# Performance work log

Measured on AMD Instinct MI355X. Metric: run time of the kernel, lower is better.

The kernel has to match this reference:

```python
import jax, jax.numpy as jnp
import numpy as np

B, T, F = 32, 128, 128      # batch, time, num_features
NF = 8                      # num_filters
KW = 5                      # kernel_width
NC = F * NF                 # num_cells = 1024
NCLS = 1000                 # num_classes
PAD = KW // 2
EPS = 1e-5


def setup_inputs() -> dict:
    key = jax.random.key(0)
    ks = jax.random.split(key, 12)
    rn = lambda k, shape, s=1.0: jax.random.normal(k, shape, dtype=jnp.float32) * s
    st = (B, NF, 1, NC)
    zc = lambda: jnp.zeros((NF,), jnp.float32)
    oc = lambda: jnp.ones((NF,), jnp.float32)
    inp = {
        "x": rn(ks[0], (B, T, F)),
        "s": rn(ks[1], st),                       # init=1.0 -> std 1 normal
        "n": jnp.zeros(st, jnp.float32),
        "d": jnp.zeros(st, jnp.float32),
        "h": jnp.zeros(st, jnp.float32),
        "a_max": jnp.full(st, -1e38, jnp.float32),  # torch fills a_max with -1e38
        "x_resize_w": rn(ks[2], (NC, F), 0.05),     # Linear(num_features->num_cells), no bias
        "g_w": rn(ks[3], (NF, NF + 1, 1, KW), 0.1), "g_b": zc(), "g_gamma": oc(), "g_beta": zc(),
        "u_w": rn(ks[4], (NF, 1, 1, KW), 0.1),      "u_b": zc(), "u_gamma": oc(), "u_beta": zc(),
        "a_w": rn(ks[5], (NF, NF + 1, 1, KW), 0.1), "a_b": zc(), "a_gamma": oc(), "a_beta": zc(),
        "dec_w": rn(ks[6], (NF, NF + 1, 1, KW), 0.1), "dec_b": zc(), "dec_gamma": oc(), "dec_beta": zc(),
        "o_w": rn(ks[7], (NCLS, NC * NF), 0.01),
        "o_b": jnp.zeros((NCLS,), jnp.float32),
    }
    return inp


def _conv(x, w, b):
    # x: [B, C_in, 1, NC]; w: [C_out, C_in, 1, KW]; 'same' padding on width (kw odd)
    y = jax.lax.conv_general_dilated(x, w, window_strides=(1, 1),
                                     padding=[(0, 0), (PAD, PAD)],
                                     dimension_numbers=("NCHW", "OIHW", "NCHW"))
    return y + b[None, :, None, None]


def _bn(x, gamma, beta):
    # BatchNorm2d in training mode: per-channel batch stats over (N, H, W), biased var
    mu = jnp.mean(x, axis=(0, 2, 3), keepdims=True)
    var = jnp.mean((x - mu) ** 2, axis=(0, 2, 3), keepdims=True)
    return gamma[None, :, None, None] * (x - mu) * jax.lax.rsqrt(var + EPS) + beta[None, :, None, None]


def reference(x, s, n, d, h, a_max,
              x_resize_w,
              g_w, g_b, g_gamma, g_beta,
              u_w, u_b, u_gamma, u_beta,
              a_w, a_b, a_gamma, a_beta,
              dec_w, dec_b, dec_gamma, dec_beta,
              o_w, o_b):
    h0 = h + jnp.tanh(s)

    def step(carry, x_t):
        h_t, n_t, d_t, am = carry
        xr = (x_t @ x_resize_w.T)[:, None, None, :]    # [B,1,1,NC]
        xh = jnp.concatenate([xr, h_t], axis=1)        # [B,NF+1,1,NC]
        g_t = _bn(_conv(xh, g_w, g_b), g_gamma, g_beta)
        u_t = _bn(_conv(xr, u_w, u_b), u_gamma, u_beta)
        a_t = _bn(_conv(xh, a_w, a_b), a_gamma, a_beta)
        dec = jax.nn.sigmoid(_bn(_conv(xh, dec_w, dec_b), dec_gamma, dec_beta))
        ed = jnp.exp(-dec)
        z_t = u_t * jnp.tanh(g_t)
        a_new = jnp.maximum(am * ed, a_t)              # torch: max(a_max*exp(-decay), a_t)
        exp_diff = jnp.exp(am - a_new)
        exp_scaled = jnp.exp(a_t - a_new)
        n_new = n_t * ed * exp_diff + z_t * exp_scaled
        d_new = d_t * ed * exp_diff + exp_scaled
        h_new = jnp.tanh(n_new / d_new)
        return (h_new, n_new, d_new, a_new), None

    (h_T, n_T, d_T, am_T), _ = jax.lax.scan(step, (h0, n, d, a_max), jnp.swapaxes(x, 0, 1))
    outs = h_T.reshape(h_T.shape[0], -1) @ o_w.T + o_b  # [B, NCLS]
    return (outs, s, n_T, d_T, h_T, am_T)
```

## Files before the change

kernel.cpp:

```cpp
#include <hip/hip_runtime.h>


#define NBLK 256
#define NTHR 512

constexpr int Bb = 32, Tt = 128, NCc = 1024;
constexpr int PROW = 1032;
constexpr float EPSf  = 1e-5f;
constexpr float INV_N = 1.0f / 32768.0f;

constexpr size_t XR_OFF  = 0;
constexpr size_t XR_SZ   = (size_t)Tt * Bb * PROW;
constexpr size_t WT_OFF  = XR_OFF + XR_SZ;
constexpr size_t WT_SZ   = 131072;
constexpr size_t WPK_OFF = WT_OFF + WT_SZ;
constexpr size_t WPK_SZ  = 1280;
constexpr size_t ACC_OFF = WPK_OFF + WPK_SZ;
constexpr size_t ACC_SZ  = 3 * 4 * 64 * 32;
constexpr size_t SL2_OFF = ACC_OFF + ACC_SZ;
constexpr size_t SL2_SZ  = 2 * 32 * 8 * 2 * 64;
constexpr size_t CNT_OFF = SL2_OFF + SL2_SZ;

constexpr int OUT_S  = 32000;
constexpr int OUT_N  = 294144;
constexpr int OUT_D  = 556288;
constexpr int OUT_H  = 818432;
constexpr int OUT_AM = 1080576;

__device__ __forceinline__ float fast_tanh(float x) {
  float e = __expf(2.0f * x);
  return 1.0f - 2.0f / (e + 1.0f);
}

__global__ void prep_kernel(const float* __restrict__ w, float* __restrict__ wT,
                            const float* __restrict__ gw, const float* __restrict__ aw,
                            const float* __restrict__ dw, const float* __restrict__ uw,
                            float* __restrict__ wpack, float* __restrict__ acc3,
                            unsigned* __restrict__ cnt) {
  const int g = blockIdx.x * 256 + threadIdx.x;
  if (g < 131072) {
    const int c = g >> 7, k = g & 127;
    wT[k * 1024 + c] = w[g];
  }
  if (g < 1280) {
    const int f = g / 160, r = g % 160, ci = r >> 4, k = r & 15;
    float v = 0.f;
    if (ci < 9) {
      if (k < 5)       v = gw[(f * 9 + ci) * 5 + k];
      else if (k < 10) v = aw[(f * 9 + ci) * 5 + (k - 5)];
      else if (k < 15) v = dw[(f * 9 + ci) * 5 + (k - 10)];
    } else {
      if (k < 5)       v = uw[f * 5 + k];
    }
    wpack[g] = v;
  }
  if (g < (int)ACC_SZ) acc3[g] = 0.f;
  if (g < 1024) cnt[g] = 0u;
}

__global__ void __launch_bounds__(256) xr_kernel(const float* __restrict__ x,
                                                 const float* __restrict__ wT,
                                                 float* __restrict__ XR) {
  const int tb0 = blockIdx.x * 16;
  const int c0  = threadIdx.x * 4;
  float4 acc[16];
#pragma unroll
  for (int j = 0; j < 16; ++j) acc[j] = make_float4(0.f, 0.f, 0.f, 0.f);
#pragma unroll 4
  for (int k = 0; k < 128; ++k) {
    const float4 wv = *(const float4*)(wT + (size_t)k * 1024 + c0);
#pragma unroll
    for (int j = 0; j < 16; ++j) {
      const int tb = tb0 + j;
      const float xs = x[(size_t)(tb & 31) * 16384 + (size_t)(tb >> 5) * 128 + k];
      acc[j].x = fmaf(xs, wv.x, acc[j].x);
      acc[j].y = fmaf(xs, wv.y, acc[j].y);
      acc[j].z = fmaf(xs, wv.z, acc[j].z);
      acc[j].w = fmaf(xs, wv.w, acc[j].w);
    }
  }
#pragma unroll
  for (int j = 0; j < 16; ++j) {
    float* row = XR + (size_t)(tb0 + j) * PROW;
    *(float4*)(row + 4 + c0) = acc[j];
    if (threadIdx.x == 0)   { row[0] = row[1] = row[2] = row[3] = 0.f; }
    if (threadIdx.x == 255) { row[1028] = row[1029] = row[1030] = row[1031] = 0.f; }
  }
}

__global__ void __launch_bounds__(NTHR) scan_kernel(
    const float* __restrict__ XR, const float* __restrict__ wpack,
    float* acc3, float* slots2, unsigned* cnt,
    const float* __restrict__ s_in, const float* __restrict__ n_in,
    const float* __restrict__ d_in, const float* __restrict__ h_in,
    const float* __restrict__ am_in,
    const float* __restrict__ ggm, const float* __restrict__ gbt,
    const float* __restrict__ ugm, const float* __restrict__ ubt,
    const float* __restrict__ agm, const float* __restrict__ abt,
    const float* __restrict__ dgm, const float* __restrict__ dbt,
    float* __restrict__ out)
{
  const int bb   = (int)blockIdx.x >> 3;
  const int cc   = (int)blockIdx.x & 7;
  const int tid  = (int)threadIdx.x;
  const int w    = tid >> 6;
  const int lane = tid & 63;
  const int fu   = __builtin_amdgcn_readfirstlane(w);
  const float* __restrict__ wpk = wpack + fu * 160;

  const int c0   = 2 * lane;
  const int gc0  = cc * 128 + c0;
  const int cellbase = bb * 8192 + w * 1024 + gc0;
  const int rep  = (int)blockIdx.x & 3;

  const float ggamma = ggm[fu], gbeta = gbt[fu];
  const float ugamma = ugm[fu], ubeta = ubt[fu];
  const float agamma = agm[fu], abeta = abt[fu];
  const float dgamma = dgm[fu], dbeta = dbt[fu];

  __shared__ float hl[8][136];

  float nst[2], dst[2], amst[2], hv[2];
  float hn = 0.f, hd = 0.f, ham = -1e38f;
  const int  hloc   = (lane < 2) ? (lane - 2) : (128 + (lane - 2));
  const bool hvalid = (lane < 4) && ((lane < 2) ? (cc > 0) : (cc < 7));
  {
    const float2 n2 = *(const float2*)(n_in  + cellbase);
    const float2 d2 = *(const float2*)(d_in  + cellbase);
    const float2 a2 = *(const float2*)(am_in + cellbase);
    const float2 h2 = *(const float2*)(h_in  + cellbase);
    const float2 s2 = *(const float2*)(s_in  + cellbase);
    nst[0] = n2.x; nst[1] = n2.y;
    dst[0] = d2.x; dst[1] = d2.y;
    amst[0] = a2.x; amst[1] = a2.y;
    hv[0] = h2.x + fast_tanh(s2.x);
    hv[1] = h2.y + fast_tanh(s2.y);
    *(float2*)&hl[w][c0 + 4] = make_float2(hv[0], hv[1]);

    float hh0 = 0.f;
    if (hvalid) {
      const int gcell = bb * 8192 + w * 1024 + cc * 128 + hloc;
      hn  = n_in[gcell]; hd = d_in[gcell]; ham = am_in[gcell];
      hh0 = h_in[gcell] + fast_tanh(s_in[gcell]);
    }
    if (lane < 4) hl[w][hloc + 4] = hh0;
    if (lane >= 4 && lane < 8) {
      const int pidx = (lane == 4) ? 0 : (lane == 5) ? 1 : (lane == 6) ? 134 : 135;
      hl[w][pidx] = 0.f;
    }
  }
  __syncthreads();

  for (int t = 0; t < Tt; ++t) {
    const int p2 = t & 1;
    const int p3 = t % 3;

    float accg[2] = {0.f, 0.f}, acca[2] = {0.f, 0.f};
    float accd[2] = {0.f, 0.f}, accu[2] = {0.f, 0.f};

    const float2* xr2 = (const float2*)(XR + (size_t)(t * Bb + bb) * PROW + 2 + gc0);
    const float2 xa = xr2[0], xb = xr2[1], xc = xr2[2];

#pragma unroll
    for (int r = 0; r < 8; ++r) {
      const float2 qa = *(const float2*)&hl[r][c0 + 2];
      const float2 qb = *(const float2*)&hl[r][c0 + 4];
      const float2 qc = *(const float2*)&hl[r][c0 + 6];
      const float w6[6] = {qa.x, qa.y, qb.x, qb.y, qc.x, qc.y};
      const float* wp = wpk + (r + 1) * 16;
#pragma unroll
      for (int kw = 0; kw < 5; ++kw) {
        const float wg = wp[kw], wa = wp[5 + kw], wd = wp[10 + kw];
#pragma unroll
        for (int j = 0; j < 2; ++j) {
          const float v = w6[j + kw];
          accg[j] = fmaf(v, wg, accg[j]);
          acca[j] = fmaf(v, wa, acca[j]);
          accd[j] = fmaf(v, wd, accd[j]);
        }
      }
    }
    {
      const float w6[6] = {xa.x, xa.y, xb.x, xb.y, xc.x, xc.y};
      const float* wp = wpk;
      const float* wu = wpk + 144;
#pragma unroll
      for (int kw = 0; kw < 5; ++kw) {
        const float wg = wp[kw], wa = wp[5 + kw], wd = wp[10 + kw], wv = wu[kw];
#pragma unroll
        for (int j = 0; j < 2; ++j) {
          const float v = w6[j + kw];
          accg[j] = fmaf(v, wg, accg[j]);
          acca[j] = fmaf(v, wa, acca[j]);
          accd[j] = fmaf(v, wd, accd[j]);
          accu[j] = fmaf(v, wv, accu[j]);
        }
      }
    }

    {
      float ps[8];
      ps[0] = accg[0] + accg[1]; ps[1] = fmaf(accg[0], accg[0], accg[1] * accg[1]);
      ps[2] = acca[0] + acca[1]; ps[3] = fmaf(acca[0], acca[0], acca[1] * acca[1]);
      ps[4] = accd[0] + accd[1]; ps[5] = fmaf(accd[0], accd[0], accd[1] * accd[1]);
      ps[6] = accu[0] + accu[1]; ps[7] = fmaf(accu[0], accu[0], accu[1] * accu[1]);
#pragma unroll
      for (int k = 0; k < 8; ++k) {
        float v = ps[k];
#pragma unroll
        for (int m = 1; m <= 32; m <<= 1) v += __shfl_xor(v, m);
        ps[k] = v;
      }
      float myv = ps[0];
#pragma unroll
      for (int k = 1; k < 8; ++k) if (lane == k) myv = ps[k];
      if (lane < 8)
        __hip_atomic_fetch_add(acc3 + p3 * 8192 + rep * 2048 + (w * 8 + lane) * 32,
                               myv, __ATOMIC_RELAXED, __HIP_MEMORY_SCOPE_AGENT);
    }

    if (lane == 0 || lane == 63) {
      const int side = lane ? 1 : 0;
      float* bs = slots2 + ((((size_t)p2 * 32 + bb) * 8 + cc) * 2 + side) * 64 + w * 8;
      __hip_atomic_store(bs + 0, accg[0], __ATOMIC_RELAXED, __HIP_MEMORY_SCOPE_AGENT);
      __hip_atomic_store(bs + 1, accg[1], __ATOMIC_RELAXED, __HIP_MEMORY_SCOPE_AGENT);
      __hip_atomic_store(bs + 2, acca[0], __ATOMIC_RELAXED, __HIP_MEMORY_SCOPE_AGENT);
      __hip_atomic_store(bs + 3, acca[1], __ATOMIC_RELAXED, __HIP_MEMORY_SCOPE_AGENT);
      __hip_atomic_store(bs + 4, accd[0], __ATOMIC_RELAXED, __HIP_MEMORY_SCOPE_AGENT);
      __hip_atomic_store(bs + 5, accd[1], __ATOMIC_RELAXED, __HIP_MEMORY_SCOPE_AGENT);
      __hip_atomic_store(bs + 6, accu[0], __ATOMIC_RELAXED, __HIP_MEMORY_SCOPE_AGENT);
      __hip_atomic_store(bs + 7, accu[1], __ATOMIC_RELAXED, __HIP_MEMORY_SCOPE_AGENT);
    }

    asm volatile("s_waitcnt vmcnt(0)" ::: "memory");
    __syncthreads();
    if (tid == 0) {
      unsigned* leaf = cnt + ((blockIdx.x >> 4) * 32);
      unsigned* root = cnt + 16 * 32;
      unsigned* gen  = cnt + 17 * 32;
      const unsigned tgt = (unsigned)(t + 1);
      const unsigned old =
          __hip_atomic_fetch_add(leaf, 1u, __ATOMIC_RELAXED, __HIP_MEMORY_SCOPE_AGENT);
      if (old == 16u * tgt - 1u) {
        const unsigned old2 =
            __hip_atomic_fetch_add(root, 1u, __ATOMIC_RELAXED, __HIP_MEMORY_SCOPE_AGENT);
        if (old2 == 16u * tgt - 1u)
          __hip_atomic_store(gen, tgt, __ATOMIC_RELAXED, __HIP_MEMORY_SCOPE_AGENT);
      }
      while (__hip_atomic_load(gen, __ATOMIC_RELAXED, __HIP_MEMORY_SCOPE_AGENT) < tgt)
        __builtin_amdgcn_s_sleep(1);
    }
    __syncthreads();

    float st[8];
    {
      float sv = 0.f;
      if (lane < 8) {
        const float* ap = acc3 + p3 * 8192 + (w * 8 + lane) * 32;
#pragma unroll
        for (int r = 0; r < 4; ++r)
          sv += __hip_atomic_load(ap + r * 2048, __ATOMIC_RELAXED, __HIP_MEMORY_SCOPE_AGENT);
      }
#pragma unroll
      for (int k = 0; k < 8; ++k) st[k] = __shfl(sv, k);
    }
    if (blockIdx.x == 0 && tid < 256)
      __hip_atomic_store(acc3 + ((t + 2) % 3) * 8192 + tid * 32, 0.f,
                         __ATOMIC_RELAXED, __HIP_MEMORY_SCOPE_AGENT);

    const float mg = st[0] * INV_N; const float vg = fmaf(-mg, mg, st[1] * INV_N);
    const float sg = ggamma * rsqrtf(vg + EPSf); const float og = fmaf(-mg, sg, gbeta);
    const float ma = st[2] * INV_N; const float va = fmaf(-ma, ma, st[3] * INV_N);
    const float sa = agamma * rsqrtf(va + EPSf); const float oa = fmaf(-ma, sa, abeta);
    const float md = st[4] * INV_N; const float vd = fmaf(-md, md, st[5] * INV_N);
    const float sd = dgamma * rsqrtf(vd + EPSf); const float od = fmaf(-md, sd, dbeta);
    const float mu = st[6] * INV_N; const float vu = fmaf(-mu, mu, st[7] * INV_N);
    const float su = ugamma * rsqrtf(vu + EPSf); const float ou = fmaf(-mu, su, ubeta);

#pragma unroll
    for (int j = 0; j < 2; ++j) {
      const float gb = fmaf(accg[j], sg, og);
      const float ab = fmaf(acca[j], sa, oa);
      const float db = fmaf(accd[j], sd, od);
      const float ub = fmaf(accu[j], su, ou);
      const float dec = 1.0f / (1.0f + __expf(-db));
      const float ed  = __expf(-dec);
      const float z   = ub * fast_tanh(gb);
      const float anew = fmaxf(amst[j] * ed, ab);
      const float e1 = __expf(amst[j] - anew);
      const float e2 = __expf(ab - anew);
      const float ede1 = ed * e1;
      nst[j]  = fmaf(nst[j], ede1, z * e2);
      dst[j]  = fmaf(dst[j], ede1, e2);
      amst[j] = anew;
      hv[j]   = fast_tanh(nst[j] / dst[j]);
    }
    *(float2*)&hl[w][c0 + 4] = make_float2(hv[0], hv[1]);

    if (lane < 4) {
      float hres = 0.f;
      if (hvalid) {
        const int ncc  = (lane < 2) ? (cc - 1) : (cc + 1);
        const int nsid = (lane < 2) ? 1 : 0;
        const float* nb =
            slots2 + ((((size_t)p2 * 32 + bb) * 8 + ncc) * 2 + nsid) * 64 + w * 8 + (lane & 1);
        const float graw = __hip_atomic_load(nb + 0, __ATOMIC_RELAXED, __HIP_MEMORY_SCOPE_AGENT);
        const float araw = __hip_atomic_load(nb + 2, __ATOMIC_RELAXED, __HIP_MEMORY_SCOPE_AGENT);
        const float draw = __hip_atomic_load(nb + 4, __ATOMIC_RELAXED, __HIP_MEMORY_SCOPE_AGENT);
        const float uraw = __hip_atomic_load(nb + 6, __ATOMIC_RELAXED, __HIP_MEMORY_SCOPE_AGENT);
        const float gb = fmaf(graw, sg, og);
        const float ab = fmaf(araw, sa, oa);
        const float db = fmaf(draw, sd, od);
        const float ub = fmaf(uraw, su, ou);
        const float dec = 1.0f / (1.0f + __expf(-db));
        const float ed  = __expf(-dec);
        const float z   = ub * fast_tanh(gb);
        const float anew = fmaxf(ham * ed, ab);
        const float e1 = __expf(ham - anew);
        const float e2 = __expf(ab - anew);
        const float ede1 = ed * e1;
        hn  = fmaf(hn, ede1, z * e2);
        hd  = fmaf(hd, ede1, e2);
        ham = anew;
        hres = fast_tanh(hn / hd);
      }
      hl[w][hloc + 4] = hres;
    }
    __syncthreads();
  }

  {
    const float2 s2 = *(const float2*)(s_in + cellbase);
    *(float2*)(out + OUT_S  + cellbase) = s2;
    *(float2*)(out + OUT_N  + cellbase) = make_float2(nst[0], nst[1]);
    *(float2*)(out + OUT_D  + cellbase) = make_float2(dst[0], dst[1]);
    *(float2*)(out + OUT_H  + cellbase) = make_float2(hv[0], hv[1]);
    *(float2*)(out + OUT_AM + cellbase) = make_float2(amst[0], amst[1]);
  }
}

__global__ void __launch_bounds__(256) out_kernel(const float* __restrict__ outH,
                                                  const float* __restrict__ ow,
                                                  const float* __restrict__ ob,
                                                  float* __restrict__ out) {
  const int g = blockIdx.x * 256 + threadIdx.x;
  const int o = g >> 5;
  const int b = g & 31;
  const float* hp = outH + (size_t)b * 8192;
  const float* wp = ow + (size_t)o * 8192;
  float acc = 0.f;
#pragma unroll 8
  for (int c = 0; c < 8192; c += 4) {
    const float4 hv4 = *(const float4*)(hp + c);
    const float4 wv4 = *(const float4*)(wp + c);
    acc = fmaf(hv4.x, wv4.x, acc);
    acc = fmaf(hv4.y, wv4.y, acc);
    acc = fmaf(hv4.z, wv4.z, acc);
    acc = fmaf(hv4.w, wv4.w, acc);
  }
  out[b * 1000 + o] = acc + ob[o];
}

extern "C" void kernel_launch(void* const* d_in, const int* in_sizes, int n_in,
                              void* d_out, int out_size, void* d_ws, size_t ws_size,
                              hipStream_t stream) {
  (void)in_sizes; (void)n_in; (void)out_size; (void)ws_size;
  const float* x   = (const float*)d_in[0];
  const float* s   = (const float*)d_in[1];
  const float* n_  = (const float*)d_in[2];
  const float* dd  = (const float*)d_in[3];
  const float* h   = (const float*)d_in[4];
  const float* am  = (const float*)d_in[5];
  const float* xrw = (const float*)d_in[6];
  const float* gw  = (const float*)d_in[7];
  const float* ggm = (const float*)d_in[9];
  const float* gbt = (const float*)d_in[10];
  const float* uw  = (const float*)d_in[11];
  const float* ugm = (const float*)d_in[13];
  const float* ubt = (const float*)d_in[14];
  const float* aw  = (const float*)d_in[15];
  const float* agm = (const float*)d_in[17];
  const float* abt = (const float*)d_in[18];
  const float* dw  = (const float*)d_in[19];
  const float* dgm = (const float*)d_in[21];
  const float* dbt = (const float*)d_in[22];
  const float* ow  = (const float*)d_in[23];
  const float* ob  = (const float*)d_in[24];
  float* out = (float*)d_out;
  float* ws  = (float*)d_ws;

  float* XR     = ws + XR_OFF;
  float* wT     = ws + WT_OFF;
  float* wpack  = ws + WPK_OFF;
  float* acc3   = ws + ACC_OFF;
  float* slots2 = ws + SL2_OFF;
  unsigned* cnt = (unsigned*)(ws + CNT_OFF);

  prep_kernel<<<dim3(512), dim3(256), 0, stream>>>(xrw, wT, gw, aw, dw, uw, wpack, acc3, cnt);
  xr_kernel<<<dim3(256), dim3(256), 0, stream>>>(x, wT, XR);

  void* args[] = { &XR, &wpack, &acc3, &slots2, &cnt, &s, &n_, &dd, &h, &am,
                   &ggm, &gbt, &ugm, &ubt, &agm, &abt, &dgm, &dbt, &out };
  hipError_t err = hipLaunchCooperativeKernel((void*)scan_kernel, dim3(NBLK), dim3(NTHR),
                                              args, 0, stream);
  if (err != hipSuccess) {
    scan_kernel<<<dim3(NBLK), dim3(NTHR), 0, stream>>>(XR, wpack, acc3, slots2, cnt,
                                                       s, n_, dd, h, am,
                                                       ggm, gbt, ugm, ubt, agm, abt,
                                                       dgm, dbt, out);
  }

  out_kernel<<<dim3(125), dim3(256), 0, stream>>>(out + OUT_H, ow, ob, out);
}
```

Measured before the change: 1.459 ms.

## Flatten grid barrier, prefetch next-step inputs, and parallelize output projection

The two-level leaf/root/generation grid barrier is replaced by four counters, one per replica. Each block increments its own counter and then polls all four. The next timestep's XR slice is prefetched before the barrier, and neighbour halo values are loaded right after it. Other changes in the scan loop: the BN-stat shuffle reduction is rewritten as a transpose-style reduction with fewer shuffles, boundary slot stores are packed into 64-bit atomics, and zeroing of the accumulator ring is spread across all blocks instead of block 0. The output GEMV is rewritten so each of 1000 blocks handles one class and reuses its weight row across all 32 batch rows. The risk is more polling traffic on four shared counters in exchange for fewer serialized barrier hops.

```diff
diff --git a/kernel.cpp b/kernel.cpp
--- a/kernel.cpp
+++ b/kernel.cpp
@@ -30,6 +30,11 @@
 __device__ __forceinline__ float fast_tanh(float x) {
   float e = __expf(2.0f * x);
   return 1.0f - 2.0f / (e + 1.0f);
+}
+
+__device__ __forceinline__ unsigned long long pack2(float a, float b) {
+  return (unsigned long long)__float_as_uint(a) |
+         ((unsigned long long)__float_as_uint(b) << 32);
 }
 
 __global__ void prep_kernel(const float* __restrict__ w, float* __restrict__ wT,
@@ -112,6 +117,7 @@
   const int gc0  = cc * 128 + c0;
   const int cellbase = bb * 8192 + w * 1024 + gc0;
   const int rep  = (int)blockIdx.x & 3;
+  const int zline = (int)blockIdx.x >> 2;
 
   const float ggamma = ggm[fu], gbeta = gbt[fu];
   const float ugamma = ugm[fu], ubeta = ubt[fu];
@@ -149,6 +155,12 @@
       hl[w][pidx] = 0.f;
     }
   }
+
+  float2 xa, xb, xc;
+  {
+    const float2* xr2 = (const float2*)(XR + (size_t)bb * PROW + 2 + gc0);
+    xa = xr2[0]; xb = xr2[1]; xc = xr2[2];
+  }
   __syncthreads();
 
   for (int t = 0; t < Tt; ++t) {
@@ -157,9 +169,6 @@
 
     float accg[2] = {0.f, 0.f}, acca[2] = {0.f, 0.f};
     float accd[2] = {0.f, 0.f}, accu[2] = {0.f, 0.f};
-
-    const float2* xr2 = (const float2*)(XR + (size_t)(t * Bb + bb) * PROW + 2 + gc0);
-    const float2 xa = xr2[0], xb = xr2[1], xc = xr2[2];
 
 #pragma unroll
     for (int r = 0; r < 8; ++r) {
@@ -205,68 +214,82 @@
       ps[4] = accd[0] + accd[1]; ps[5] = fmaf(accd[0], accd[0], accd[1] * accd[1]);
       ps[6] = accu[0] + accu[1]; ps[7] = fmaf(accu[0], accu[0], accu[1] * accu[1]);
 #pragma unroll
-      for (int k = 0; k < 8; ++k) {
-        float v = ps[k];
-#pragma unroll
-        for (int m = 1; m <= 32; m <<= 1) v += __shfl_xor(v, m);
-        ps[k] = v;
-      }
-      float myv = ps[0];
-#pragma unroll
-      for (int k = 1; k < 8; ++k) if (lane == k) myv = ps[k];
+      for (int m = 1; m <= 4; m <<= 1)
+#pragma unroll
+        for (int k = 0; k < 8; ++k) ps[k] += __shfl_xor(ps[k], m);
+      const int l3 = lane & 7;
+      const float a0 = (l3 & 1) ? ps[1] : ps[0];
+      const float a1 = (l3 & 1) ? ps[3] : ps[2];
+      const float a2 = (l3 & 1) ? ps[5] : ps[4];
+      const float a3 = (l3 & 1) ? ps[7] : ps[6];
+      const float b0 = (l3 & 2) ? a1 : a0;
+      const float b1 = (l3 & 2) ? a3 : a2;
+      float v = (l3 & 4) ? b1 : b0;
+#pragma unroll
+      for (int m = 8; m <= 32; m <<= 1) v += __shfl_xor(v, m);
       if (lane < 8)
         __hip_atomic_fetch_add(acc3 + p3 * 8192 + rep * 2048 + (w * 8 + lane) * 32,
-                               myv, __ATOMIC_RELAXED, __HIP_MEMORY_SCOPE_AGENT);
+                               v, __ATOMIC_RELAXED, __HIP_MEMORY_SCOPE_AGENT);
     }
 
     if (lane == 0 || lane == 63) {
       const int side = lane ? 1 : 0;
-      float* bs = slots2 + ((((size_t)p2 * 32 + bb) * 8 + cc) * 2 + side) * 64 + w * 8;
-      __hip_atomic_store(bs + 0, accg[0], __ATOMIC_RELAXED, __HIP_MEMORY_SCOPE_AGENT);
-      __hip_atomic_store(bs + 1, accg[1], __ATOMIC_RELAXED, __HIP_MEMORY_SCOPE_AGENT);
-      __hip_atomic_store(bs + 2, acca[0], __ATOMIC_RELAXED, __HIP_MEMORY_SCOPE_AGENT);
-      __hip_atomic_store(bs + 3, acca[1], __ATOMIC_RELAXED, __HIP_MEMORY_SCOPE_AGENT);
-      __hip_atomic_store(bs + 4, accd[0], __ATOMIC_RELAXED, __HIP_MEMORY_SCOPE_AGENT);
-      __hip_atomic_store(bs + 5, accd[1], __ATOMIC_RELAXED, __HIP_MEMORY_SCOPE_AGENT);
-      __hip_atomic_store(bs + 6, accu[0], __ATOMIC_RELAXED, __HIP_MEMORY_SCOPE_AGENT);
-      __hip_atomic_store(bs + 7, accu[1], __ATOMIC_RELAXED, __HIP_MEMORY_SCOPE_AGENT);
+      unsigned long long* bs = (unsigned long long*)
+          (slots2 + ((((size_t)p2 * 32 + bb) * 8 + cc) * 2 + side) * 64 + w * 8);
+      __hip_atomic_store(bs + 0, pack2(accg[0], accg[1]), __ATOMIC_RELAXED, __HIP_MEMORY_SCOPE_AGENT);
+      __hip_atomic_store(bs + 1, pack2(acca[0], acca[1]), __ATOMIC_RELAXED, __HIP_MEMORY_SCOPE_AGENT);
+      __hip_atomic_store(bs + 2, pack2(accd[0], accd[1]), __ATOMIC_RELAXED, __HIP_MEMORY_SCOPE_AGENT);
+      __hip_atomic_store(bs + 3, pack2(accu[0], accu[1]), __ATOMIC_RELAXED, __HIP_MEMORY_SCOPE_AGENT);
+    }
+
+    float2 nxa, nxb, nxc;
+    {
+      const int tn = (t + 1 < Tt) ? (t + 1) : t;
+      const float2* xr2 = (const float2*)(XR + (size_t)(tn * Bb + bb) * PROW + 2 + gc0);
+      nxa = xr2[0]; nxb = xr2[1]; nxc = xr2[2];
     }
 
     asm volatile("s_waitcnt vmcnt(0)" ::: "memory");
     __syncthreads();
     if (tid == 0) {
-      unsigned* leaf = cnt + ((blockIdx.x >> 4) * 32);
-      unsigned* root = cnt + 16 * 32;
-      unsigned* gen  = cnt + 17 * 32;
-      const unsigned tgt = (unsigned)(t + 1);
-      const unsigned old =
-          __hip_atomic_fetch_add(leaf, 1u, __ATOMIC_RELAXED, __HIP_MEMORY_SCOPE_AGENT);
-      if (old == 16u * tgt - 1u) {
-        const unsigned old2 =
-            __hip_atomic_fetch_add(root, 1u, __ATOMIC_RELAXED, __HIP_MEMORY_SCOPE_AGENT);
-        if (old2 == 16u * tgt - 1u)
-          __hip_atomic_store(gen, tgt, __ATOMIC_RELAXED, __HIP_MEMORY_SCOPE_AGENT);
+      __hip_atomic_fetch_add(cnt + rep * 32, 1u, __ATOMIC_RELAXED, __HIP_MEMORY_SCOPE_AGENT);
+      const unsigned tgt = 64u * (unsigned)(t + 1);
+      while (true) {
+        const unsigned c0_ = __hip_atomic_load(cnt +  0, __ATOMIC_RELAXED, __HIP_MEMORY_SCOPE_AGENT);
+        const unsigned c1_ = __hip_atomic_load(cnt + 32, __ATOMIC_RELAXED, __HIP_MEMORY_SCOPE_AGENT);
+        const unsigned c2_ = __hip_atomic_load(cnt + 64, __ATOMIC_RELAXED, __HIP_MEMORY_SCOPE_AGENT);
+        const unsigned c3_ = __hip_atomic_load(cnt + 96, __ATOMIC_RELAXED, __HIP_MEMORY_SCOPE_AGENT);
+        if (c0_ >= tgt && c1_ >= tgt && c2_ >= tgt && c3_ >= tgt) break;
+        __builtin_amdgcn_s_sleep(2);
       }
-      while (__hip_atomic_load(gen, __ATOMIC_RELAXED, __HIP_MEMORY_SCOPE_AGENT) < tgt)
-        __builtin_amdgcn_s_sleep(1);
     }
     __syncthreads();
 
+    float v = 0.f;
+    if (lane < 8) {
+      const float* ap = acc3 + p3 * 8192 + (w * 8 + lane) * 32;
+#pragma unroll
+      for (int r = 0; r < 4; ++r)
+        v += __hip_atomic_load(ap + r * 2048, __ATOMIC_RELAXED, __HIP_MEMORY_SCOPE_AGENT);
+    }
+    float graw = 0.f, araw = 0.f, draw = 0.f, uraw = 0.f;
+    if (hvalid) {
+      const int ncc  = (lane < 2) ? (cc - 1) : (cc + 1);
+      const int nsid = (lane < 2) ? 1 : 0;
+      const float* nb =
+          slots2 + ((((size_t)p2 * 32 + bb) * 8 + ncc) * 2 + nsid) * 64 + w * 8 + (lane & 1);
+      graw = __hip_atomic_load(nb + 0, __ATOMIC_RELAXED, __HIP_MEMORY_SCOPE_AGENT);
+      araw = __hip_atomic_load(nb + 2, __ATOMIC_RELAXED, __HIP_MEMORY_SCOPE_AGENT);
+      draw = __hip_atomic_load(nb + 4, __ATOMIC_RELAXED, __HIP_MEMORY_SCOPE_AGENT);
+      uraw = __hip_atomic_load(nb + 6, __ATOMIC_RELAXED, __HIP_MEMORY_SCOPE_AGENT);
+    }
+    if (tid == 256)
+      __hip_atomic_store(acc3 + ((t + 2) % 3) * 8192 + rep * 2048 + zline * 32, 0.f,
+                         __ATOMIC_RELAXED, __HIP_MEMORY_SCOPE_AGENT);
+
     float st[8];
-    {
-      float sv = 0.f;
-      if (lane < 8) {
-        const float* ap = acc3 + p3 * 8192 + (w * 8 + lane) * 32;
-#pragma unroll
-        for (int r = 0; r < 4; ++r)
-          sv += __hip_atomic_load(ap + r * 2048, __ATOMIC_RELAXED, __HIP_MEMORY_SCOPE_AGENT);
-      }
-#pragma unroll
-      for (int k = 0; k < 8; ++k) st[k] = __shfl(sv, k);
-    }
-    if (blockIdx.x == 0 && tid < 256)
-      __hip_atomic_store(acc3 + ((t + 2) % 3) * 8192 + tid * 32, 0.f,
-                         __ATOMIC_RELAXED, __HIP_MEMORY_SCOPE_AGENT);
+#pragma unroll
+    for (int k = 0; k < 8; ++k) st[k] = __shfl(v, k);
 
     const float mg = st[0] * INV_N; const float vg = fmaf(-mg, mg, st[1] * INV_N);
     const float sg = ggamma * rsqrtf(vg + EPSf); const float og = fmaf(-mg, sg, gbeta);
@@ -300,14 +323,6 @@
     if (lane < 4) {
       float hres = 0.f;
       if (hvalid) {
-        const int ncc  = (lane < 2) ? (cc - 1) : (cc + 1);
-        const int nsid = (lane < 2) ? 1 : 0;
-        const float* nb =
-            slots2 + ((((size_t)p2 * 32 + bb) * 8 + ncc) * 2 + nsid) * 64 + w * 8 + (lane & 1);
-        const float graw = __hip_atomic_load(nb + 0, __ATOMIC_RELAXED, __HIP_MEMORY_SCOPE_AGENT);
-        const float araw = __hip_atomic_load(nb + 2, __ATOMIC_RELAXED, __HIP_MEMORY_SCOPE_AGENT);
-        const float draw = __hip_atomic_load(nb + 4, __ATOMIC_RELAXED, __HIP_MEMORY_SCOPE_AGENT);
-        const float uraw = __hip_atomic_load(nb + 6, __ATOMIC_RELAXED, __HIP_MEMORY_SCOPE_AGENT);
         const float gb = fmaf(graw, sg, og);
         const float ab = fmaf(araw, sa, oa);
         const float db = fmaf(draw, sd, od);
@@ -327,6 +342,8 @@
       hl[w][hloc + 4] = hres;
     }
     __syncthreads();
+
+    xa = nxa; xb = nxb; xc = nxc;
   }
 
   {
@@ -343,22 +360,42 @@
                                                   const float* __restrict__ ow,
                                                   const float* __restrict__ ob,
                                                   float* __restrict__ out) {
-  const int g = blockIdx.x * 256 + threadIdx.x;
-  const int o = g >> 5;
-  const int b = g & 31;
-  const float* hp = outH + (size_t)b * 8192;
-  const float* wp = ow + (size_t)o * 8192;
-  float acc = 0.f;
-#pragma unroll 8
-  for (int c = 0; c < 8192; c += 4) {
-    const float4 hv4 = *(const float4*)(hp + c);
-    const float4 wv4 = *(const float4*)(wp + c);
-    acc = fmaf(hv4.x, wv4.x, acc);
-    acc = fmaf(hv4.y, wv4.y, acc);
-    acc = fmaf(hv4.z, wv4.z, acc);
-    acc = fmaf(hv4.w, wv4.w, acc);
-  }
-  out[b * 1000 + o] = acc + ob[o];
+  const int o   = blockIdx.x;
+  const int tid = (int)threadIdx.x;
+  const int wv  = tid >> 6;
+  const int lane = tid & 63;
+
+  float4 wr[8];
+  {
+    const float4* wq = (const float4*)(ow + (size_t)o * 8192 + tid * 32);
+#pragma unroll
+    for (int k = 0; k < 8; ++k) wr[k] = wq[k];
+  }
+  float acc[32];
+#pragma unroll
+  for (int b = 0; b < 32; ++b) {
+    const float4* hq = (const float4*)(outH + (size_t)b * 8192 + tid * 32);
+    float s0 = 0.f, s1 = 0.f;
+#pragma unroll
+    for (int k = 0; k < 8; k += 2) {
+      const float4 h0 = hq[k], h1 = hq[k + 1];
+      s0 = fmaf(h0.x, wr[k].x, s0);     s0 = fmaf(h0.y, wr[k].y, s0);
+      s0 = fmaf(h0.z, wr[k].z, s0);     s0 = fmaf(h0.w, wr[k].w, s0);
+      s1 = fmaf(h1.x, wr[k+1].x, s1);   s1 = fmaf(h1.y, wr[k+1].y, s1);
+      s1 = fmaf(h1.z, wr[k+1].z, s1);   s1 = fmaf(h1.w, wr[k+1].w, s1);
+    }
+    acc[b] = s0 + s1;
+  }
+#pragma unroll
+  for (int m = 1; m <= 32; m <<= 1)
+#pragma unroll
+    for (int b = 0; b < 32; ++b) acc[b] += __shfl_xor(acc[b], m);
+
+  __shared__ float red[4][32];
+  if (lane < 32) red[wv][lane] = acc[lane];
+  __syncthreads();
+  if (tid < 32)
+    out[tid * 1000 + o] = red[0][tid] + red[1][tid] + red[2][tid] + red[3][tid] + ob[o];
 }
 
 extern "C" void kernel_launch(void* const* d_in, const int* in_sizes, int n_in,
@@ -410,5 +447,5 @@
                                                        dgm, dbt, out);
   }
 
-  out_kernel<<<dim3(125), dim3(256), 0, stream>>>(out + OUT_H, ow, ob, out);
-}
+  out_kernel<<<dim3(1000), dim3(256), 0, stream>>>(out + OUT_H, ow, ob, out);
+}
```

New measurement: 1.484 ms. No clear change (+1.7%).
